# Kernel optimization log

Hardware: AMD Instinct MI355X
Metric: run time of the kernel (lower is better)

Reference implementation:

```python
import math
import jax, jax.numpy as jnp
import numpy as np

B, S, D_MODEL, H = 2, 2048, 1024, 16
HEAD_DIM = D_MODEL // H
NUM_BUCKETS = 32
MAX_DISTANCE = 128
SCALING = HEAD_DIM ** (-0.5)


def setup_inputs() -> dict:
    key = jax.random.key(0)
    ks = jax.random.split(key, 6)
    inp = {
        "hidden_states": jax.random.normal(ks[0], (B, S, D_MODEL), jnp.float32),
        "Wq": jax.random.normal(ks[1], (D_MODEL, D_MODEL), jnp.float32) * (D_MODEL ** -0.5),
        "Wk": jax.random.normal(ks[2], (D_MODEL, D_MODEL), jnp.float32) * (D_MODEL ** -0.5),
        "Wv": jax.random.normal(ks[3], (D_MODEL, D_MODEL), jnp.float32) * (D_MODEL ** -0.5),
        "Wo": jax.random.normal(ks[4], (D_MODEL, D_MODEL), jnp.float32) * (D_MODEL ** -0.5),
        "rel_emb": jax.random.normal(ks[5], (NUM_BUCKETS, H), jnp.float32),
    }
    return inp


def _relative_position_bucket(relative_position, num_buckets=NUM_BUCKETS, max_distance=MAX_DISTANCE):
    # bidirectional (encoder) bucketing, matches T5 _relative_position_bucket
    num_buckets = num_buckets // 2
    relative_buckets = (relative_position > 0).astype(jnp.int32) * num_buckets
    relative_position = jnp.abs(relative_position)
    max_exact = num_buckets // 2
    is_small = relative_position < max_exact
    rp_f = jnp.maximum(relative_position, 1).astype(jnp.float32)  # guard log(0)
    rel_if_large = max_exact + (
        jnp.log(rp_f / max_exact) / math.log(max_distance / max_exact) * (num_buckets - max_exact)
    ).astype(jnp.int32)
    rel_if_large = jnp.minimum(rel_if_large, num_buckets - 1)
    relative_buckets = relative_buckets + jnp.where(is_small, relative_position, rel_if_large)
    return relative_buckets


def compute_bias(rel_emb, q_len, k_len):
    context_position = jnp.arange(q_len)[:, None]
    memory_position = jnp.arange(k_len)[None, :]
    relative_position = memory_position - context_position  # [q, k]
    buckets = _relative_position_bucket(relative_position)
    values = rel_emb[buckets]                  # [q, k, H]
    return jnp.transpose(values, (2, 0, 1))[None]  # [1, H, q, k]


def reference(hidden_states, Wq, Wk, Wv, Wo, rel_emb):
    b, s, _ = hidden_states.shape

    def shape(x):  # [b, s, d_model] -> [b, H, s, head_dim]
        return x.reshape(b, s, H, HEAD_DIM).transpose(0, 2, 1, 3)

    q = shape(hidden_states @ Wq.T)
    k = shape(hidden_states @ Wk.T)
    v = shape(hidden_states @ Wv.T)

    position_bias = compute_bias(rel_emb, s, s)            # [1, H, s, s]
    scores = jnp.einsum("bhqd,bhkd->bhqk", q, k) * SCALING + position_bias
    attn = jax.nn.softmax(scores, axis=-1)
    ctx = jnp.einsum("bhqk,bhkd->bhqd", attn, v)           # [b, H, s, head_dim]
    ctx = ctx.transpose(0, 2, 1, 3).reshape(b, s, D_MODEL)
    return ctx @ Wo.T
```

## Files before the change

### kernel.cpp

```cpp
#include <hip/hip_runtime.h>
#include <math.h>

#define H_    16
#define S_    2048
#define DH_   64
#define DM_   1024
#define NTOK_ 4096
#define NBIAS_ 4095

typedef __attribute__((ext_vector_type(8))) short short8;
typedef __attribute__((ext_vector_type(4))) float f32x4;

#define MFMA16(a, b, c) __builtin_amdgcn_mfma_f32_16x16x32_bf16((a), (b), (c), 0, 0, 0)

__device__ __forceinline__ ushort f2bf(float f) {
  union { float f; unsigned u; } x; x.f = f;
  unsigned r = (x.u + 0x7FFFu + ((x.u >> 16) & 1u)) >> 16;
  return (ushort)r;
}
__device__ __forceinline__ ushort f2bf_fast(float f) {
  union { float f; unsigned u; } x; x.f = f;
  return (ushort)((x.u + 0x8000u) >> 16);
}

__device__ __forceinline__ void ldg16_lds(const ushort* g, ushort* l) {
  __builtin_amdgcn_global_load_lds(
      (const __attribute__((address_space(1))) unsigned int*)g,
      (__attribute__((address_space(3))) unsigned int*)l, 16, 0, 0);
}

__global__ void cast_bf16_k(const float* __restrict__ in, ushort* __restrict__ out, int n) {
  int i = (blockIdx.x * blockDim.x + threadIdx.x) * 4;
  if (i >= n) return;
  const float4 v = *(const float4*)(in + i);
  ushort4 o;
  o.x = f2bf(v.x); o.y = f2bf(v.y); o.z = f2bf(v.z); o.w = f2bf(v.w);
  *(ushort4*)(out + i) = o;
}

__global__ void build_bias_k(const float* __restrict__ rel_emb, float* __restrict__ biasTab) {
  int d = blockIdx.x * blockDim.x + threadIdx.x;
  if (d >= NBIAS_) return;
  int rp = d - (S_ - 1);
  int ret = (rp > 0) ? 16 : 0;
  int arp = rp < 0 ? -rp : rp;
  int bucket;
  if (arp < 8) {
    bucket = ret + arp;
  } else {
    float t = logf((float)arp * 0.125f);
    t = t / 2.772588722239781f;
    t = t * 8.0f;
    int large = 8 + (int)t;
    if (large > 15) large = 15;
    bucket = ret + large;
  }
  for (int h = 0; h < H_; ++h)
    biasTab[h * NBIAS_ + d] = rel_emb[bucket * H_ + h];
}

__global__ __launch_bounds__(256) void gemm_qkv_k(
    const ushort* __restrict__ X,
    const ushort* __restrict__ Wq, const ushort* __restrict__ Wk, const ushort* __restrict__ Wv,
    ushort* __restrict__ Q, ushort* __restrict__ K, ushort* __restrict__ Vt)
{
  const int z = blockIdx.z;
  const ushort* __restrict__ W = (z == 0) ? Wq : (z == 1) ? Wk : Wv;
  __shared__ __align__(16) ushort As[128 * 32];
  __shared__ __align__(16) ushort Bs[128 * 32];

  const int tid = threadIdx.x;
  const int wave = tid >> 6, lane = tid & 63;
  const int l15 = lane & 15, l4 = lane >> 4;
  const int wm = wave >> 1, wn = wave & 1;
  const int m0 = blockIdx.y * 128;
  const int n0 = blockIdx.x * 128;
  const int srow = lane >> 2, scol = (lane & 3) * 8;

  f32x4 acc[4][4];
#pragma unroll
  for (int mi = 0; mi < 4; ++mi)
#pragma unroll
    for (int ni = 0; ni < 4; ++ni) acc[mi][ni] = (f32x4){0.f, 0.f, 0.f, 0.f};

  for (int k0 = 0; k0 < DM_; k0 += 32) {
    __syncthreads();
#pragma unroll
    for (int i = 0; i < 4; ++i) {
      int c = wave * 4 + i;
      if (c < 8)
        ldg16_lds(X + (size_t)(m0 + c * 16 + srow) * DM_ + k0 + scol, &As[c * 512]);
      else
        ldg16_lds(W + (size_t)(n0 + (c - 8) * 16 + srow) * DM_ + k0 + scol, &Bs[(c - 8) * 512]);
    }
    __syncthreads();
    short8 af[4], bfr[4];
#pragma unroll
    for (int mi = 0; mi < 4; ++mi)
      af[mi] = *(const short8*)&As[(wm * 64 + mi * 16 + l15) * 32 + l4 * 8];
#pragma unroll
    for (int ni = 0; ni < 4; ++ni)
      bfr[ni] = *(const short8*)&Bs[(wn * 64 + ni * 16 + l15) * 32 + l4 * 8];
#pragma unroll
    for (int mi = 0; mi < 4; ++mi)
#pragma unroll
      for (int ni = 0; ni < 4; ++ni)
        acc[mi][ni] = MFMA16(af[mi], bfr[ni], acc[mi][ni]);
  }

#pragma unroll
  for (int mi = 0; mi < 4; ++mi)
#pragma unroll
    for (int ni = 0; ni < 4; ++ni)
#pragma unroll
      for (int r = 0; r < 4; ++r) {
        int m = m0 + wm * 64 + mi * 16 + l4 * 4 + r;
        int n = n0 + wn * 64 + ni * 16 + l15;
        int b = m >> 11, s = m & (S_ - 1);
        int h = n >> 6, d = n & 63;
        ushort bv = f2bf(acc[mi][ni][r]);
        if (z == 0)      Q [((size_t)(b * H_ + h) * S_ + s) * DH_ + d] = bv;
        else if (z == 1) K [((size_t)(b * H_ + h) * S_ + s) * DH_ + d] = bv;
        else             Vt[((size_t)(b * H_ + h) * DH_ + d) * S_ + s] = bv;
      }
}

__global__ __launch_bounds__(256) void gemm_out_k(
    const ushort* __restrict__ A, const ushort* __restrict__ W, float* __restrict__ out)
{
  __shared__ __align__(16) ushort As[128 * 32];
  __shared__ __align__(16) ushort Bs[128 * 32];
  const int tid = threadIdx.x;
  const int wave = tid >> 6, lane = tid & 63;
  const int l15 = lane & 15, l4 = lane >> 4;
  const int wm = wave >> 1, wn = wave & 1;
  const int m0 = blockIdx.y * 128;
  const int n0 = blockIdx.x * 128;
  const int srow = lane >> 2, scol = (lane & 3) * 8;

  f32x4 acc[4][4];
#pragma unroll
  for (int mi = 0; mi < 4; ++mi)
#pragma unroll
    for (int ni = 0; ni < 4; ++ni) acc[mi][ni] = (f32x4){0.f, 0.f, 0.f, 0.f};

  for (int k0 = 0; k0 < DM_; k0 += 32) {
    __syncthreads();
#pragma unroll
    for (int i = 0; i < 4; ++i) {
      int c = wave * 4 + i;
      if (c < 8)
        ldg16_lds(A + (size_t)(m0 + c * 16 + srow) * DM_ + k0 + scol, &As[c * 512]);
      else
        ldg16_lds(W + (size_t)(n0 + (c - 8) * 16 + srow) * DM_ + k0 + scol, &Bs[(c - 8) * 512]);
    }
    __syncthreads();
    short8 af[4], bfr[4];
#pragma unroll
    for (int mi = 0; mi < 4; ++mi)
      af[mi] = *(const short8*)&As[(wm * 64 + mi * 16 + l15) * 32 + l4 * 8];
#pragma unroll
    for (int ni = 0; ni < 4; ++ni)
      bfr[ni] = *(const short8*)&Bs[(wn * 64 + ni * 16 + l15) * 32 + l4 * 8];
#pragma unroll
    for (int mi = 0; mi < 4; ++mi)
#pragma unroll
      for (int ni = 0; ni < 4; ++ni)
        acc[mi][ni] = MFMA16(af[mi], bfr[ni], acc[mi][ni]);
  }

#pragma unroll
  for (int mi = 0; mi < 4; ++mi)
#pragma unroll
    for (int ni = 0; ni < 4; ++ni)
#pragma unroll
      for (int r = 0; r < 4; ++r) {
        int m = m0 + wm * 64 + mi * 16 + l4 * 4 + r;
        int n = n0 + wn * 64 + ni * 16 + l15;
        out[(size_t)m * DM_ + n] = acc[mi][ni][r];
      }
}

__global__ __launch_bounds__(256, 4) void attn_k(
    const ushort* __restrict__ Q, const ushort* __restrict__ K, const ushort* __restrict__ Vt,
    const float* __restrict__ biasTab, ushort* __restrict__ Ctx)
{
  __shared__ float brev[2112];
  __shared__ __align__(16) ushort Ks[2][64][32];
  __shared__ __align__(16) ushort Vs[2][64][32];
  __shared__ __align__(16) ushort Ps[4][16 * 72];

  const int tid = threadIdx.x;
  const int wave = tid >> 6, lane = tid & 63;
  const int l15 = lane & 15, l4 = lane >> 4;
  const int bh = blockIdx.y;
  const int h = bh & (H_ - 1);
  const int b = bh >> 4;
  const int qb = blockIdx.x * 64;
  const int q0 = qb + wave * 16;
  const int srow = lane >> 2, scol = (lane & 3) * 8;

  for (int j = tid; j < 2111; j += 256) brev[j] = biasTab[h * NBIAS_ + (4094 - j - qb)];

  const ushort* Qh = Q  + (size_t)bh * S_ * DH_;
  const ushort* Kh = K  + (size_t)bh * S_ * DH_;
  const ushort* Vh = Vt + (size_t)bh * DH_ * S_;

  short8 qf[2];
#pragma unroll
  for (int kk = 0; kk < 2; ++kk)
    qf[kk] = *(const short8*)(Qh + (size_t)(q0 + l15) * DH_ + kk * 32 + l4 * 8);

  short8 ones;
#pragma unroll
  for (int i = 0; i < 8; ++i) ones[i] = (short)0x3F80;

  f32x4 of[4];
#pragma unroll
  for (int nt = 0; nt < 4; ++nt) of[nt] = (f32x4){0.f, 0.f, 0.f, 0.f};
  f32x4 ls = (f32x4){0.f, 0.f, 0.f, 0.f};

  ushort* Pw = &Ps[wave][0];
  const int jb0 = 2047 + wave * 16 + l4 * 4 - l15;

  for (int kt = 0; kt < S_; kt += 64) {
    __syncthreads();
#pragma unroll
    for (int i = 0; i < 2; ++i) {
      int c = wave * 2 + i;
      int kk = c >> 2, rg = c & 3;
      ldg16_lds(Kh + (size_t)(kt + rg * 16 + srow) * DH_ + kk * 32 + scol,
                &Ks[0][0][0] + c * 512);
      ldg16_lds(Vh + (size_t)(rg * 16 + srow) * S_ + kt + kk * 32 + scol,
                &Vs[0][0][0] + c * 512);
    }
    __syncthreads();

    f32x4 sc[4];
#pragma unroll
    for (int nt = 0; nt < 4; ++nt) sc[nt] = (f32x4){0.f, 0.f, 0.f, 0.f};
#pragma unroll
    for (int kk = 0; kk < 2; ++kk)
#pragma unroll
      for (int nt = 0; nt < 4; ++nt) {
        short8 kf = *(const short8*)&Ks[kk][nt * 16 + l15][l4 * 8];
        sc[nt] = MFMA16(qf[kk], kf, sc[nt]);
      }

#pragma unroll
    for (int nt = 0; nt < 4; ++nt) {
      const int jb = jb0 - kt - nt * 16;
#pragma unroll
      for (int r = 0; r < 4; ++r) {
        float p = __expf(sc[nt][r] * 0.125f + brev[jb + r]);
        Pw[(l4 * 4 + r) * 72 + nt * 16 + l15] = f2bf_fast(p);
      }
    }

#pragma unroll
    for (int kk = 0; kk < 2; ++kk) {
      short8 pf = *(const short8*)&Pw[l15 * 72 + kk * 32 + l4 * 8];
      ls = MFMA16(pf, ones, ls);
#pragma unroll
      for (int nt = 0; nt < 4; ++nt) {
        short8 vf = *(const short8*)&Vs[kk][nt * 16 + l15][l4 * 8];
        of[nt] = MFMA16(pf, vf, of[nt]);
      }
    }
  }

#pragma unroll
  for (int nt = 0; nt < 4; ++nt)
#pragma unroll
    for (int r = 0; r < 4; ++r) {
      int t = b * S_ + q0 + l4 * 4 + r;
      float v = of[nt][r] / ls[r];
      Ctx[(size_t)t * DM_ + h * 64 + nt * 16 + l15] = f2bf(v);
    }
}

extern "C" void kernel_launch(void* const* d_in, const int* in_sizes, int n_in,
                              void* d_out, int out_size, void* d_ws, size_t ws_size,
                              hipStream_t stream) {
  const float* hs  = (const float*)d_in[0];
  const float* Wq  = (const float*)d_in[1];
  const float* Wk  = (const float*)d_in[2];
  const float* Wv  = (const float*)d_in[3];
  const float* Wo  = (const float*)d_in[4];
  const float* rel = (const float*)d_in[5];
  float* out = (float*)d_out;

  ushort* Xb  = (ushort*)d_ws;
  ushort* Wqb = Xb  + (size_t)NTOK_ * DM_;
  ushort* Wkb = Wqb + (size_t)DM_ * DM_;
  ushort* Wvb = Wkb + (size_t)DM_ * DM_;
  ushort* Wob = Wvb + (size_t)DM_ * DM_;
  ushort* Qd  = Wob + (size_t)DM_ * DM_;
  ushort* Kd  = Qd  + (size_t)NTOK_ * DM_;
  ushort* Vtd = Kd  + (size_t)NTOK_ * DM_;
  float* biasTab = (float*)(Vtd + (size_t)NTOK_ * DM_);
  ushort* Ctx = Xb;

  cast_bf16_k<<<4096, 256, 0, stream>>>(hs, Xb, NTOK_ * DM_);
  cast_bf16_k<<<1024, 256, 0, stream>>>(Wq, Wqb, DM_ * DM_);
  cast_bf16_k<<<1024, 256, 0, stream>>>(Wk, Wkb, DM_ * DM_);
  cast_bf16_k<<<1024, 256, 0, stream>>>(Wv, Wvb, DM_ * DM_);
  cast_bf16_k<<<1024, 256, 0, stream>>>(Wo, Wob, DM_ * DM_);
  build_bias_k<<<16, 256, 0, stream>>>(rel, biasTab);

  gemm_qkv_k<<<dim3(8, 32, 3), 256, 0, stream>>>(Xb, Wqb, Wkb, Wvb, Qd, Kd, Vtd);
  attn_k<<<dim3(S_ / 64, 2 * H_), 256, 0, stream>>>(Qd, Kd, Vtd, biasTab, Ctx);
  gemm_out_k<<<dim3(8, 32), 256, 0, stream>>>(Ctx, Wob, out);
}
```

Baseline: 233.4 us.

## Swizzle LDS tiles, deepen GEMM K-step, and split attention keys across waves

The shared GEMM loop now stages a K-slice of 64 per iteration into XOR-swizzled LDS rows to cut bank conflicts and halve barrier count. The V projection is transposed through LDS so Vt is written with 16-byte coalesced stores instead of scattered 2-byte writes. The attention kernel is restructured: each wave handles 16 keys for all 64 queries, computing S^T so P stays in registers (half-zeroed MFMA operands) and no LDS round-trip is needed. Partial outputs and row sums are then reduced across waves through LDS at the end. The trade-off is wasted MFMA work from zero-padded operands, a serial cross-wave reduction, and lower occupancy (launch bound of 2).

```diff
diff --git a/kernel.cpp b/kernel.cpp
--- a/kernel.cpp
+++ b/kernel.cpp
@@ -59,23 +59,62 @@
     biasTab[h * NBIAS_ + d] = rel_emb[bucket * H_ + h];
 }
 
+__device__ __forceinline__ void gemm_core(
+    const ushort* __restrict__ gA, const ushort* __restrict__ gB,
+    ushort* As, ushort* Bs, f32x4 (&acc)[4][4],
+    int m0, int n0, int wave, int lane)
+{
+  const int l15 = lane & 15, quad = lane >> 4;
+  const int wm = wave >> 1, wn = wave & 1;
+  const int srow = lane >> 3;
+  const int sw = ((lane & 7) ^ (lane >> 3)) * 8;
+  const int px = l15 & 7;
+
+  for (int k0 = 0; k0 < DM_; k0 += 64) {
+    __syncthreads();
+#pragma unroll
+    for (int i = 0; i < 8; ++i) {
+      int c = wave * 8 + i;
+      if (c < 16)
+        ldg16_lds(gA + (size_t)(m0 + c * 8 + srow) * DM_ + k0 + sw, As + c * 512);
+      else
+        ldg16_lds(gB + (size_t)(n0 + (c - 16) * 8 + srow) * DM_ + k0 + sw, Bs + (c - 16) * 512);
+    }
+    __syncthreads();
+#pragma unroll
+    for (int kk = 0; kk < 2; ++kk) {
+      short8 af[4], bfr[4];
+#pragma unroll
+      for (int mi = 0; mi < 4; ++mi)
+        af[mi] = *(const short8*)&As[(wm * 64 + mi * 16 + l15) * 64 + (((kk * 4 + quad) ^ px)) * 8];
+#pragma unroll
+      for (int ni = 0; ni < 4; ++ni)
+        bfr[ni] = *(const short8*)&Bs[(wn * 64 + ni * 16 + l15) * 64 + (((kk * 4 + quad) ^ px)) * 8];
+#pragma unroll
+      for (int mi = 0; mi < 4; ++mi)
+#pragma unroll
+        for (int ni = 0; ni < 4; ++ni)
+          acc[mi][ni] = MFMA16(af[mi], bfr[ni], acc[mi][ni]);
+    }
+  }
+}
+
 __global__ __launch_bounds__(256) void gemm_qkv_k(
     const ushort* __restrict__ X,
     const ushort* __restrict__ Wq, const ushort* __restrict__ Wk, const ushort* __restrict__ Wv,
     ushort* __restrict__ Q, ushort* __restrict__ K, ushort* __restrict__ Vt)
 {
+  __shared__ __align__(16) ushort sh[17408];
+  ushort* As = sh;
+  ushort* Bs = sh + 8192;
   const int z = blockIdx.z;
   const ushort* __restrict__ W = (z == 0) ? Wq : (z == 1) ? Wk : Wv;
-  __shared__ __align__(16) ushort As[128 * 32];
-  __shared__ __align__(16) ushort Bs[128 * 32];
-
   const int tid = threadIdx.x;
   const int wave = tid >> 6, lane = tid & 63;
-  const int l15 = lane & 15, l4 = lane >> 4;
+  const int l15 = lane & 15, quad = lane >> 4;
   const int wm = wave >> 1, wn = wave & 1;
   const int m0 = blockIdx.y * 128;
   const int n0 = blockIdx.x * 128;
-  const int srow = lane >> 2, scol = (lane & 3) * 8;
 
   f32x4 acc[4][4];
 #pragma unroll
@@ -83,60 +122,60 @@
 #pragma unroll
     for (int ni = 0; ni < 4; ++ni) acc[mi][ni] = (f32x4){0.f, 0.f, 0.f, 0.f};
 
-  for (int k0 = 0; k0 < DM_; k0 += 32) {
-    __syncthreads();
-#pragma unroll
-    for (int i = 0; i < 4; ++i) {
-      int c = wave * 4 + i;
-      if (c < 8)
-        ldg16_lds(X + (size_t)(m0 + c * 16 + srow) * DM_ + k0 + scol, &As[c * 512]);
-      else
-        ldg16_lds(W + (size_t)(n0 + (c - 8) * 16 + srow) * DM_ + k0 + scol, &Bs[(c - 8) * 512]);
-    }
-    __syncthreads();
-    short8 af[4], bfr[4];
+  gemm_core(X, W, As, Bs, acc, m0, n0, wave, lane);
+
+  if (z < 2) {
+    ushort* dst = (z == 0) ? Q : K;
 #pragma unroll
     for (int mi = 0; mi < 4; ++mi)
-      af[mi] = *(const short8*)&As[(wm * 64 + mi * 16 + l15) * 32 + l4 * 8];
-#pragma unroll
-    for (int ni = 0; ni < 4; ++ni)
-      bfr[ni] = *(const short8*)&Bs[(wn * 64 + ni * 16 + l15) * 32 + l4 * 8];
+#pragma unroll
+      for (int ni = 0; ni < 4; ++ni)
+#pragma unroll
+        for (int r = 0; r < 4; ++r) {
+          int m = m0 + wm * 64 + mi * 16 + quad * 4 + r;
+          int n = n0 + wn * 64 + ni * 16 + l15;
+          int b = m >> 11, s = m & (S_ - 1);
+          int hh = n >> 6, dd = n & 63;
+          dst[((size_t)(b * H_ + hh) * S_ + s) * DH_ + dd] = f2bf(acc[mi][ni][r]);
+        }
+  } else {
+    __syncthreads();
 #pragma unroll
     for (int mi = 0; mi < 4; ++mi)
 #pragma unroll
-      for (int ni = 0; ni < 4; ++ni)
-        acc[mi][ni] = MFMA16(af[mi], bfr[ni], acc[mi][ni]);
-  }
-
-#pragma unroll
-  for (int mi = 0; mi < 4; ++mi)
-#pragma unroll
-    for (int ni = 0; ni < 4; ++ni)
-#pragma unroll
-      for (int r = 0; r < 4; ++r) {
-        int m = m0 + wm * 64 + mi * 16 + l4 * 4 + r;
-        int n = n0 + wn * 64 + ni * 16 + l15;
-        int b = m >> 11, s = m & (S_ - 1);
-        int h = n >> 6, d = n & 63;
-        ushort bv = f2bf(acc[mi][ni][r]);
-        if (z == 0)      Q [((size_t)(b * H_ + h) * S_ + s) * DH_ + d] = bv;
-        else if (z == 1) K [((size_t)(b * H_ + h) * S_ + s) * DH_ + d] = bv;
-        else             Vt[((size_t)(b * H_ + h) * DH_ + d) * S_ + s] = bv;
+      for (int ni = 0; ni < 4; ++ni) {
+        int n = wn * 64 + ni * 16 + l15;
+        int m = wm * 64 + mi * 16 + quad * 4;
+        ushort4 w4;
+        w4.x = f2bf(acc[mi][ni][0]); w4.y = f2bf(acc[mi][ni][1]);
+        w4.z = f2bf(acc[mi][ni][2]); w4.w = f2bf(acc[mi][ni][3]);
+        *(ushort4*)&sh[n * 136 + m] = w4;
       }
+    __syncthreads();
+    const int b = m0 >> 11, s0 = m0 & (S_ - 1);
+#pragma unroll
+    for (int p = 0; p < 8; ++p) {
+      int task = p * 256 + tid;
+      int n = task >> 4, mc = (task & 15) * 8;
+      int col = n0 + n, hh = col >> 6, dd = col & 63;
+      *(short8*)(Vt + ((size_t)(b * H_ + hh) * DH_ + dd) * S_ + s0 + mc) =
+          *(const short8*)&sh[n * 136 + mc];
+    }
+  }
 }
 
 __global__ __launch_bounds__(256) void gemm_out_k(
     const ushort* __restrict__ A, const ushort* __restrict__ W, float* __restrict__ out)
 {
-  __shared__ __align__(16) ushort As[128 * 32];
-  __shared__ __align__(16) ushort Bs[128 * 32];
+  __shared__ __align__(16) ushort sh[16384];
+  ushort* As = sh;
+  ushort* Bs = sh + 8192;
   const int tid = threadIdx.x;
   const int wave = tid >> 6, lane = tid & 63;
-  const int l15 = lane & 15, l4 = lane >> 4;
+  const int l15 = lane & 15, quad = lane >> 4;
   const int wm = wave >> 1, wn = wave & 1;
   const int m0 = blockIdx.y * 128;
   const int n0 = blockIdx.x * 128;
-  const int srow = lane >> 2, scol = (lane & 3) * 8;
 
   f32x4 acc[4][4];
 #pragma unroll
@@ -144,139 +183,152 @@
 #pragma unroll
     for (int ni = 0; ni < 4; ++ni) acc[mi][ni] = (f32x4){0.f, 0.f, 0.f, 0.f};
 
-  for (int k0 = 0; k0 < DM_; k0 += 32) {
-    __syncthreads();
-#pragma unroll
-    for (int i = 0; i < 4; ++i) {
-      int c = wave * 4 + i;
-      if (c < 8)
-        ldg16_lds(A + (size_t)(m0 + c * 16 + srow) * DM_ + k0 + scol, &As[c * 512]);
-      else
-        ldg16_lds(W + (size_t)(n0 + (c - 8) * 16 + srow) * DM_ + k0 + scol, &Bs[(c - 8) * 512]);
-    }
-    __syncthreads();
-    short8 af[4], bfr[4];
-#pragma unroll
-    for (int mi = 0; mi < 4; ++mi)
-      af[mi] = *(const short8*)&As[(wm * 64 + mi * 16 + l15) * 32 + l4 * 8];
+  gemm_core(A, W, As, Bs, acc, m0, n0, wave, lane);
+
+#pragma unroll
+  for (int mi = 0; mi < 4; ++mi)
 #pragma unroll
     for (int ni = 0; ni < 4; ++ni)
-      bfr[ni] = *(const short8*)&Bs[(wn * 64 + ni * 16 + l15) * 32 + l4 * 8];
-#pragma unroll
-    for (int mi = 0; mi < 4; ++mi)
-#pragma unroll
-      for (int ni = 0; ni < 4; ++ni)
-        acc[mi][ni] = MFMA16(af[mi], bfr[ni], acc[mi][ni]);
-  }
-
-#pragma unroll
-  for (int mi = 0; mi < 4; ++mi)
-#pragma unroll
-    for (int ni = 0; ni < 4; ++ni)
 #pragma unroll
       for (int r = 0; r < 4; ++r) {
-        int m = m0 + wm * 64 + mi * 16 + l4 * 4 + r;
+        int m = m0 + wm * 64 + mi * 16 + quad * 4 + r;
         int n = n0 + wn * 64 + ni * 16 + l15;
         out[(size_t)m * DM_ + n] = acc[mi][ni][r];
       }
 }
 
-__global__ __launch_bounds__(256, 4) void attn_k(
+__global__ __launch_bounds__(256, 2) void attn_k(
     const ushort* __restrict__ Q, const ushort* __restrict__ K, const ushort* __restrict__ Vt,
     const float* __restrict__ biasTab, ushort* __restrict__ Ctx)
 {
-  __shared__ float brev[2112];
-  __shared__ __align__(16) ushort Ks[2][64][32];
-  __shared__ __align__(16) ushort Vs[2][64][32];
-  __shared__ __align__(16) ushort Ps[4][16 * 72];
+  __shared__ __align__(16) ushort KV[8192];
+  __shared__ float bias_s[2111];
+  ushort* Ks = KV;
+  ushort* Vs = KV + 4096;
 
   const int tid = threadIdx.x;
   const int wave = tid >> 6, lane = tid & 63;
-  const int l15 = lane & 15, l4 = lane >> 4;
+  const int l15 = lane & 15, quad = lane >> 4;
   const int bh = blockIdx.y;
   const int h = bh & (H_ - 1);
   const int b = bh >> 4;
   const int qb = blockIdx.x * 64;
-  const int q0 = qb + wave * 16;
-  const int srow = lane >> 2, scol = (lane & 3) * 8;
-
-  for (int j = tid; j < 2111; j += 256) brev[j] = biasTab[h * NBIAS_ + (4094 - j - qb)];
+  const int srow = lane >> 3;
+  const int sw = ((lane & 7) ^ (lane >> 3)) * 8;
+
+  const f32x4 zero4 = {0.f, 0.f, 0.f, 0.f};
+
+  for (int i = tid; i < 2111; i += 256)
+    bias_s[i] = biasTab[h * NBIAS_ + 1984 - qb + i];
 
   const ushort* Qh = Q  + (size_t)bh * S_ * DH_;
   const ushort* Kh = K  + (size_t)bh * S_ * DH_;
   const ushort* Vh = Vt + (size_t)bh * DH_ * S_;
 
-  short8 qf[2];
-#pragma unroll
-  for (int kk = 0; kk < 2; ++kk)
-    qf[kk] = *(const short8*)(Qh + (size_t)(q0 + l15) * DH_ + kk * 32 + l4 * 8);
-
-  short8 ones;
-#pragma unroll
-  for (int i = 0; i < 8; ++i) ones[i] = (short)0x3F80;
-
-  f32x4 of[4];
-#pragma unroll
-  for (int nt = 0; nt < 4; ++nt) of[nt] = (f32x4){0.f, 0.f, 0.f, 0.f};
-  f32x4 ls = (f32x4){0.f, 0.f, 0.f, 0.f};
-
-  ushort* Pw = &Ps[wave][0];
-  const int jb0 = 2047 + wave * 16 + l4 * 4 - l15;
+  short8 qf[4][2];
+#pragma unroll
+  for (int nf = 0; nf < 4; ++nf)
+#pragma unroll
+    for (int kk = 0; kk < 2; ++kk)
+      qf[nf][kk] = *(const short8*)(Qh + (size_t)(qb + nf * 16 + l15) * DH_ + kk * 32 + quad * 8);
+
+  short8 oneh;
+#pragma unroll
+  for (int i = 0; i < 8; ++i) oneh[i] = (i < 4) ? (short)0x3F80 : (short)0;
+
+  f32x4 of[4][4];
+#pragma unroll
+  for (int nf = 0; nf < 4; ++nf)
+#pragma unroll
+    for (int nt = 0; nt < 4; ++nt) of[nf][nt] = zero4;
+  f32x4 ls[4];
+#pragma unroll
+  for (int nf = 0; nf < 4; ++nf) ls[nf] = zero4;
+
+  const int kidx = (wave * 16 + l15) * 64;
+  const int vslot = wave * 2 + (quad >> 1);
 
   for (int kt = 0; kt < S_; kt += 64) {
     __syncthreads();
 #pragma unroll
     for (int i = 0; i < 2; ++i) {
       int c = wave * 2 + i;
-      int kk = c >> 2, rg = c & 3;
-      ldg16_lds(Kh + (size_t)(kt + rg * 16 + srow) * DH_ + kk * 32 + scol,
-                &Ks[0][0][0] + c * 512);
-      ldg16_lds(Vh + (size_t)(rg * 16 + srow) * S_ + kt + kk * 32 + scol,
-                &Vs[0][0][0] + c * 512);
-    }
-    __syncthreads();
-
+      ldg16_lds(Kh + (size_t)(kt + c * 8 + srow) * DH_ + sw, Ks + c * 512);
+      ldg16_lds(Vh + (size_t)(c * 8 + srow) * S_ + kt + sw, Vs + c * 512);
+    }
+    __syncthreads();
+
+    short8 kf0 = *(const short8*)&Ks[kidx + ((quad ^ (l15 & 7))) * 8];
+    short8 kf1 = *(const short8*)&Ks[kidx + (((4 + quad) ^ (l15 & 7))) * 8];
     f32x4 sc[4];
 #pragma unroll
-    for (int nt = 0; nt < 4; ++nt) sc[nt] = (f32x4){0.f, 0.f, 0.f, 0.f};
-#pragma unroll
-    for (int kk = 0; kk < 2; ++kk)
-#pragma unroll
-      for (int nt = 0; nt < 4; ++nt) {
-        short8 kf = *(const short8*)&Ks[kk][nt * 16 + l15][l4 * 8];
-        sc[nt] = MFMA16(qf[kk], kf, sc[nt]);
+    for (int nf = 0; nf < 4; ++nf) {
+      sc[nf] = MFMA16(kf0, qf[nf][0], zero4);
+      sc[nf] = MFMA16(kf1, qf[nf][1], sc[nf]);
+    }
+
+    short8 pf[4];
+    const int ib = kt + wave * 16 + quad * 4 + 63 - l15;
+#pragma unroll
+    for (int nf = 0; nf < 4; ++nf) {
+      const int i0 = ib - nf * 16;
+      pf[nf][0] = (short)f2bf_fast(__expf(sc[nf][0] * 0.125f + bias_s[i0]));
+      pf[nf][1] = (short)f2bf_fast(__expf(sc[nf][1] * 0.125f + bias_s[i0 + 1]));
+      pf[nf][2] = (short)f2bf_fast(__expf(sc[nf][2] * 0.125f + bias_s[i0 + 2]));
+      pf[nf][3] = (short)f2bf_fast(__expf(sc[nf][3] * 0.125f + bias_s[i0 + 3]));
+      pf[nf][4] = 0; pf[nf][5] = 0; pf[nf][6] = 0; pf[nf][7] = 0;
+    }
+
+#pragma unroll
+    for (int nf = 0; nf < 4; ++nf) ls[nf] = MFMA16(pf[nf], oneh, ls[nf]);
+#pragma unroll
+    for (int nt = 0; nt < 4; ++nt) {
+      ushort4 v4 = *(const ushort4*)&Vs[(nt * 16 + l15) * 64 +
+                                        ((vslot ^ (l15 & 7))) * 8 + (quad & 1) * 4];
+      short8 vf;
+      vf[0] = (short)v4.x; vf[1] = (short)v4.y; vf[2] = (short)v4.z; vf[3] = (short)v4.w;
+      vf[4] = 0; vf[5] = 0; vf[6] = 0; vf[7] = 0;
+#pragma unroll
+      for (int nf = 0; nf < 4; ++nf)
+        of[nf][nt] = MFMA16(pf[nf], vf, of[nf][nt]);
+    }
+  }
+
+  __syncthreads();
+  float* red = (float*)KV;
+#pragma unroll 1
+  for (int mi = 0; mi < 4; ++mi) {
+    if (wave) {
+      int base = ((wave - 1) * 64 + lane) * 21;
+#pragma unroll
+      for (int nt = 0; nt < 4; ++nt)
+#pragma unroll
+        for (int r = 0; r < 4; ++r) red[base + nt * 4 + r] = of[mi][nt][r];
+#pragma unroll
+      for (int r = 0; r < 4; ++r) red[base + 16 + r] = ls[mi][r];
+    }
+    __syncthreads();
+    if (wave == 0) {
+#pragma unroll
+      for (int w = 1; w < 4; ++w) {
+        int base = ((w - 1) * 64 + lane) * 21;
+#pragma unroll
+        for (int nt = 0; nt < 4; ++nt)
+#pragma unroll
+          for (int r = 0; r < 4; ++r) of[mi][nt][r] += red[base + nt * 4 + r];
+#pragma unroll
+        for (int r = 0; r < 4; ++r) ls[mi][r] += red[base + 16 + r];
       }
-
-#pragma unroll
-    for (int nt = 0; nt < 4; ++nt) {
-      const int jb = jb0 - kt - nt * 16;
-#pragma unroll
-      for (int r = 0; r < 4; ++r) {
-        float p = __expf(sc[nt][r] * 0.125f + brev[jb + r]);
-        Pw[(l4 * 4 + r) * 72 + nt * 16 + l15] = f2bf_fast(p);
-      }
-    }
-
-#pragma unroll
-    for (int kk = 0; kk < 2; ++kk) {
-      short8 pf = *(const short8*)&Pw[l15 * 72 + kk * 32 + l4 * 8];
-      ls = MFMA16(pf, ones, ls);
-#pragma unroll
-      for (int nt = 0; nt < 4; ++nt) {
-        short8 vf = *(const short8*)&Vs[kk][nt * 16 + l15][l4 * 8];
-        of[nt] = MFMA16(pf, vf, of[nt]);
-      }
-    }
-  }
-
-#pragma unroll
-  for (int nt = 0; nt < 4; ++nt)
-#pragma unroll
-    for (int r = 0; r < 4; ++r) {
-      int t = b * S_ + q0 + l4 * 4 + r;
-      float v = of[nt][r] / ls[r];
-      Ctx[(size_t)t * DM_ + h * 64 + nt * 16 + l15] = f2bf(v);
-    }
+#pragma unroll
+      for (int nt = 0; nt < 4; ++nt)
+#pragma unroll
+        for (int r = 0; r < 4; ++r) {
+          int t = b * S_ + qb + mi * 16 + quad * 4 + r;
+          Ctx[(size_t)t * DM_ + h * 64 + nt * 16 + l15] = f2bf(of[mi][nt][r] / ls[mi][r]);
+        }
+    }
+    __syncthreads();
+  }
 }
 
 extern "C" void kernel_launch(void* const* d_in, const int* in_sizes, int n_in,
```

Result: slower. 810.0 us (+247.1%).
